# Performance work log

Measured on AMD Instinct MI355X. Metric: run time of the kernel, lower is better.

Reference implementation:

```python
import jax, jax.numpy as jnp
import numpy as np


def _causal_mask(n):
    # pixelSNAIL get_causal_mask: strict lower triangular (pixel i attends to pixels < i)
    return jnp.tril(jnp.ones((n, n), dtype=jnp.float32), k=-1)


def setup_inputs() -> dict:
    key = jax.random.key(0)
    kq, kk, kv = jax.random.split(key, 3)
    B, H, W, C, CM = 32, 32, 32, 128, 256
    return {
        "query": jax.random.normal(kq, (B, H, W, C), dtype=jnp.float32),
        "key": jax.random.normal(kk, (B, H, W, C), dtype=jnp.float32),
        "value": jax.random.normal(kv, (B, H, W, CM), dtype=jnp.float32),
    }


def reference(query, key, value):
    B = query.shape[0]
    C = key.shape[-1]
    CM = value.shape[-1]
    Nk = int(np.prod(key.shape[1:-1]))
    Nq = int(np.prod(query.shape[1:-1]))
    q = query.reshape(B, Nq, C)
    k = key.reshape(B, Nk, C)
    v = value.reshape(B, Nk, CM)
    # raw QK^T (no 1/sqrt(d) scaling in original)
    dot = jnp.einsum('bqc,bkc->bqk', q, k)
    # NON-STANDARD: softmax over full row first, then multiply by strict causal mask
    probs = jax.nn.softmax(dot, axis=-1) * _causal_mask(Nq)[None]
    mixed = jnp.einsum('bqk,bkm->bqm', probs, v)
    return mixed.reshape(query.shape[:-1] + (CM,))
```

## Files before the change

kernel.cpp:

```cpp
#include <hip/hip_runtime.h>


typedef __attribute__((ext_vector_type(8))) short short8;
typedef __attribute__((ext_vector_type(4))) float floatx4;

#define MFMA16(a, b, c) __builtin_amdgcn_mfma_f32_16x16x32_bf16((a), (b), (c), 0, 0, 0)

constexpr int N = 1024, C = 128, CM = 256, BATCH = 32;
constexpr int BM = 64;
constexpr int BN = 32;
constexpr int NT = N / BN;
constexpr int KFRAG = BN * C;
constexpr int VFRAG = BN * CM;

__device__ __forceinline__ unsigned short f2bf(float x) {
    unsigned int u = __float_as_uint(x);
    u += 0x7fffu + ((u >> 16) & 1u);
    return (unsigned short)(u >> 16);
}
__device__ __forceinline__ float bf2f(unsigned short h) {
    return __uint_as_float(((unsigned int)h) << 16);
}
__device__ __forceinline__ uint2 pack4(const unsigned short* s) {
    uint2 u;
    u.x = (unsigned)s[0] | ((unsigned)s[1] << 16);
    u.y = (unsigned)s[2] | ((unsigned)s[3] << 16);
    return u;
}
__device__ __forceinline__ void gl2lds16(const unsigned short* g, unsigned short* l) {
    __builtin_amdgcn_global_load_lds(
        (const __attribute__((address_space(1))) void*)g,
        (__attribute__((address_space(3))) void*)l, 16, 0, 0);
}

__global__ __launch_bounds__(256, 4)
void prep_kernel(const float* __restrict__ kg, const float* __restrict__ vg,
                 unsigned short* __restrict__ khi, unsigned short* __restrict__ klo,
                 unsigned short* __restrict__ vf)
{
    __shared__ __align__(16) unsigned short sKh[KFRAG];
    __shared__ __align__(16) unsigned short sKl[KFRAG];
    __shared__ __align__(16) unsigned short sV[VFRAG];

    const int tid = threadIdx.x;
    const int l = tid & 63, w = tid >> 6;
    const int tile = blockIdx.x, bat = blockIdx.y;
    const int n0 = tile * BN;
    const float* kb = kg + ((size_t)bat * N + n0) * C;
    const float* vb = vg + ((size_t)bat * N + n0) * CM;

#pragma unroll
    for (int it = 0; it < 4; ++it) {
        const int lin = tid + it * 256;
        const float4 x = *(const float4*)(kb + (size_t)lin * 4);
        const int cr = lin >> 1, h = lin & 1;
        const int slot = cr ^ ((cr >> 4) & 7);
        float xs[4] = {x.x, x.y, x.z, x.w};
        unsigned short hi[4], lo[4];
#pragma unroll
        for (int e = 0; e < 4; ++e) {
            unsigned short hb = f2bf(xs[e]);
            hi[e] = hb;
            lo[e] = f2bf(xs[e] - bf2f(hb));
        }
        *(uint2*)(&sKh[slot * 8 + h * 4]) = pack4(hi);
        *(uint2*)(&sKl[slot * 8 + h * 4]) = pack4(lo);
    }

#pragma unroll
    for (int g = 0; g < 2; ++g) {
        const int k0 = g * 16 + w * 4;
        float xa[4][4];
#pragma unroll
        for (int d = 0; d < 4; ++d) {
            const float4 t = *(const float4*)(vb + (size_t)(k0 + d) * CM + l * 4);
            xa[0][d] = t.x; xa[1][d] = t.y; xa[2][d] = t.z; xa[3][d] = t.w;
        }
        const int qq = k0 >> 3, j0 = k0 & 7;
#pragma unroll
        for (int e = 0; e < 4; ++e) {
            const int cm = l * 4 + e;
            const int ct = cm >> 4, rr = cm & 15;
            const int ch = ct * 64 + qq * 16 + rr;
            const int slot = ch ^ ((ch >> 6) & 15);
            unsigned short o[4];
#pragma unroll
            for (int d = 0; d < 4; ++d) o[d] = f2bf(xa[e][d]);
            *(uint2*)(&sV[slot * 8 + j0]) = pack4(o);
        }
    }

    __syncthreads();

    unsigned short* khb = khi + ((size_t)bat * NT + tile) * KFRAG;
    unsigned short* klb = klo + ((size_t)bat * NT + tile) * KFRAG;
    unsigned short* vfb = vf + ((size_t)bat * NT + tile) * VFRAG;

#pragma unroll
    for (int it = 0; it < 2; ++it) {
        const int oc = tid + it * 256;
        const int cr = ((oc & 15) + ((oc >> 8) << 4)) * 16 + ((oc >> 6) & 3) * 4 + ((oc >> 4) & 3);
        const int slot = cr ^ ((cr >> 4) & 7);
        *(uint4*)(khb + (size_t)oc * 8) = *(const uint4*)(&sKh[slot * 8]);
        *(uint4*)(klb + (size_t)oc * 8) = *(const uint4*)(&sKl[slot * 8]);
    }
#pragma unroll
    for (int it = 0; it < 4; ++it) {
        const int oc = tid + it * 256;
        const int slot = oc ^ ((oc >> 6) & 15);
        *(uint4*)(vfb + (size_t)oc * 8) = *(const uint4*)(&sV[slot * 8]);
    }
}

__global__ __launch_bounds__(256, 2)
void attn_kernel(const float* __restrict__ qg, float* __restrict__ og,
                 const unsigned short* __restrict__ khi,
                 const unsigned short* __restrict__ klo,
                 const unsigned short* __restrict__ vf)
{
    __shared__ __align__(16) unsigned short sKhi[2][KFRAG];
    __shared__ __align__(16) unsigned short sKlo[2][KFRAG];
    __shared__ __align__(16) unsigned short sV[2][VFRAG];

    const int tid = threadIdx.x;
    const int w = tid >> 6, ln = tid & 63;
    const int r = ln & 15, qd = ln >> 4;
    const int bat = blockIdx.x;
    const int qt = blockIdx.y;
    const int q0 = qt * BM;

    const float* qb = qg + (size_t)bat * N * C;
    float* ob = og + (size_t)bat * N * CM;
    const unsigned short* khb = khi + (size_t)bat * NT * KFRAG;
    const unsigned short* klb = klo + (size_t)bat * NT * KFRAG;
    const unsigned short* vfb = vf + (size_t)bat * NT * VFRAG;

    short8 qhi[4], qlo[4];
    {
        const float* qr = qb + (size_t)(q0 + w * 16 + r) * C + qd * 8;
#pragma unroll
        for (int ks = 0; ks < 4; ++ks) {
            float4 a = *(const float4*)(qr + ks * 32);
            float4 b = *(const float4*)(qr + ks * 32 + 4);
            float xs[8] = {a.x, a.y, a.z, a.w, b.x, b.y, b.z, b.w};
            short8 h, l;
#pragma unroll
            for (int j = 0; j < 8; ++j) {
                unsigned short hb = f2bf(xs[j]);
                h[j] = (short)hb;
                l[j] = (short)f2bf(xs[j] - bf2f(hb));
            }
            qhi[ks] = h;
            qlo[ks] = l;
        }
    }

    floatx4 oacc[16];
#pragma unroll
    for (int ct = 0; ct < 16; ++ct) oacc[ct] = (floatx4){0.f, 0.f, 0.f, 0.f};
    float lsum = 0.f;
    const int qrow = q0 + w * 16 + r;

    gl2lds16(khb + (size_t)tid * 8,         &sKhi[0][tid * 8]);
    gl2lds16(khb + (size_t)(tid + 256) * 8, &sKhi[0][(tid + 256) * 8]);
    gl2lds16(klb + (size_t)tid * 8,         &sKlo[0][tid * 8]);
    gl2lds16(klb + (size_t)(tid + 256) * 8, &sKlo[0][(tid + 256) * 8]);
#pragma unroll
    for (int i = 0; i < 4; ++i)
        gl2lds16(vfb + (size_t)(tid + i * 256) * 8, &sV[0][(tid + i * 256) * 8]);

    for (int tile = 0; tile < NT; ++tile) {
        const bool pvt = (tile <= 2 * qt + 1);
        const int cb = tile & 1;

        if (tile + 1 < NT) {
            const unsigned short* k1 = khb + (size_t)(tile + 1) * KFRAG;
            const unsigned short* l1 = klb + (size_t)(tile + 1) * KFRAG;
            unsigned short* dh = &sKhi[cb ^ 1][0];
            unsigned short* dl = &sKlo[cb ^ 1][0];
            gl2lds16(k1 + (size_t)tid * 8,         dh + tid * 8);
            gl2lds16(k1 + (size_t)(tid + 256) * 8, dh + (tid + 256) * 8);
            gl2lds16(l1 + (size_t)tid * 8,         dl + tid * 8);
            gl2lds16(l1 + (size_t)(tid + 256) * 8, dl + (tid + 256) * 8);
            if (tile + 1 <= 2 * qt + 1) {
                const unsigned short* vs = vfb + (size_t)(tile + 1) * VFRAG;
                unsigned short* dv = &sV[cb ^ 1][0];
#pragma unroll
                for (int i = 0; i < 4; ++i)
                    gl2lds16(vs + (size_t)(tid + i * 256) * 8, dv + (tid + i * 256) * 8);
                asm volatile("s_waitcnt vmcnt(8)" ::: "memory");
            } else {
                asm volatile("s_waitcnt vmcnt(4)" ::: "memory");
            }
        } else {
            asm volatile("s_waitcnt vmcnt(0)" ::: "memory");
        }
        asm volatile("s_barrier" ::: "memory");

        float pk[8];
#pragma unroll
        for (int t = 0; t < 2; ++t) {
            floatx4 a0 = (floatx4){0.f, 0.f, 0.f, 0.f};
            floatx4 a1 = (floatx4){0.f, 0.f, 0.f, 0.f};
            floatx4 a2 = (floatx4){0.f, 0.f, 0.f, 0.f};
#pragma unroll
            for (int ks = 0; ks < 4; ++ks) {
                short8 bh = *(const short8*)(&sKhi[cb][(((t * 4 + ks) * 64) + ln) * 8]);
                short8 bl = *(const short8*)(&sKlo[cb][(((t * 4 + ks) * 64) + ln) * 8]);
                a0 = MFMA16(bh, qhi[ks], a0);
                a1 = MFMA16(bh, qlo[ks], a1);
                a2 = MFMA16(bl, qhi[ks], a2);
            }
            const int kbase = tile * BN + t * 16 + qd * 4;
#pragma unroll
            for (int rg = 0; rg < 4; ++rg) {
                float s = a0[rg] + a1[rg] + a2[rg];
                float p = __expf(s - 40.0f);
                lsum += p;
                pk[t * 4 + rg] = (kbase + rg < qrow) ? p : 0.0f;
            }
        }

        if (pvt) {
            unsigned int w0, w1, w2, w3;
            asm("v_cvt_pk_bf16_f32 %0, %1, %2" : "=v"(w0) : "v"(pk[0]), "v"(pk[1]));
            asm("v_cvt_pk_bf16_f32 %0, %1, %2" : "=v"(w1) : "v"(pk[2]), "v"(pk[3]));
            asm("v_cvt_pk_bf16_f32 %0, %1, %2" : "=v"(w2) : "v"(pk[4]), "v"(pk[5]));
            asm("v_cvt_pk_bf16_f32 %0, %1, %2" : "=v"(w3) : "v"(pk[6]), "v"(pk[7]));
            asm("v_permlane32_swap_b32 %0, %1" : "+v"(w0), "+v"(w2));
            asm("v_permlane16_swap_b32 %0, %1" : "+v"(w0), "+v"(w2));
            asm("v_permlane32_swap_b32 %0, %1" : "+v"(w1), "+v"(w3));
            asm("v_permlane16_swap_b32 %0, %1" : "+v"(w1), "+v"(w3));
            uint4 apu = make_uint4(w0, w1, w2, w3);
            short8 ap = *(const short8*)&apu;
#pragma unroll
            for (int ct = 0; ct < 16; ++ct) {
                short8 bv = *(const short8*)(&sV[cb][(ct * 64 + ln) * 8]);
                oacc[ct] = MFMA16(ap, bv, oacc[ct]);
            }
        }
        asm volatile("s_barrier" ::: "memory");
    }

    float vtot = lsum;
    vtot += __shfl_xor(vtot, 16);
    vtot += __shfl_xor(vtot, 32);

#pragma unroll
    for (int rg = 0; rg < 4; ++rg) {
        float inv = 1.0f / __shfl(vtot, qd * 4 + rg);
        float* orow = ob + (size_t)(q0 + w * 16 + qd * 4 + rg) * CM;
#pragma unroll
        for (int ct = 0; ct < 16; ++ct)
            orow[ct * 16 + r] = oacc[ct][rg] * inv;
    }
}

extern "C" void kernel_launch(void* const* d_in, const int* in_sizes, int n_in,
                              void* d_out, int out_size, void* d_ws, size_t ws_size,
                              hipStream_t stream) {
    const float* q = (const float*)d_in[0];
    const float* k = (const float*)d_in[1];
    const float* v = (const float*)d_in[2];
    float* o = (float*)d_out;
    (void)n_in; (void)in_sizes; (void)out_size; (void)ws_size;

    unsigned short* khi = (unsigned short*)d_ws;
    unsigned short* klo = khi + (size_t)BATCH * NT * KFRAG;
    unsigned short* vf  = klo + (size_t)BATCH * NT * KFRAG;

    prep_kernel<<<dim3(NT, BATCH), dim3(256), 0, stream>>>(k, v, khi, klo, vf);
    attn_kernel<<<dim3(BATCH, N / BM), dim3(256), 0, stream>>>(q, o, khi, klo, vf);
}
```

Before: 151.6 us.

## Double query rows per wave to reuse K/V LDS fragments across two row groups

Raises the query tile from 64 to 128 rows, giving each wave two 16-row groups. Every K and V fragment read from LDS now feeds two MFMAs, and K/V global traffic per query row is halved because the grid has half as many blocks. The cost is twice the accumulator registers, which forces occupancy down to one block per SIMD group. The grid also drops to 256 blocks, so GPU fill and the tail effects of the causal work imbalance get worse.

New measurement: 164.4 us. +8.4%, slower.

```diff
diff --git a/kernel.cpp b/kernel.cpp
--- a/kernel.cpp
+++ b/kernel.cpp
@@ -7,7 +7,7 @@
 #define MFMA16(a, b, c) __builtin_amdgcn_mfma_f32_16x16x32_bf16((a), (b), (c), 0, 0, 0)
 
 constexpr int N = 1024, C = 128, CM = 256, BATCH = 32;
-constexpr int BM = 64;
+constexpr int BM = 128;
 constexpr int BN = 32;
 constexpr int NT = N / BN;
 constexpr int KFRAG = BN * C;
@@ -112,7 +112,7 @@
     }
 }
 
-__global__ __launch_bounds__(256, 2)
+__global__ __launch_bounds__(256, 1)
 void attn_kernel(const float* __restrict__ qg, float* __restrict__ og,
                  const unsigned short* __restrict__ khi,
                  const unsigned short* __restrict__ klo,
@@ -128,6 +128,7 @@
     const int bat = blockIdx.x;
     const int qt = blockIdx.y;
     const int q0 = qt * BM;
+    const int wrow0 = q0 + w * 32;
 
     const float* qb = qg + (size_t)bat * N * C;
     float* ob = og + (size_t)bat * N * CM;
@@ -135,9 +136,10 @@
     const unsigned short* klb = klo + (size_t)bat * NT * KFRAG;
     const unsigned short* vfb = vf + (size_t)bat * NT * VFRAG;
 
-    short8 qhi[4], qlo[4];
-    {
-        const float* qr = qb + (size_t)(q0 + w * 16 + r) * C + qd * 8;
+    short8 qhi[2][4], qlo[2][4];
+#pragma unroll
+    for (int g = 0; g < 2; ++g) {
+        const float* qr = qb + (size_t)(wrow0 + g * 16 + r) * C + qd * 8;
 #pragma unroll
         for (int ks = 0; ks < 4; ++ks) {
             float4 a = *(const float4*)(qr + ks * 32);
@@ -150,16 +152,19 @@
                 h[j] = (short)hb;
                 l[j] = (short)f2bf(xs[j] - bf2f(hb));
             }
-            qhi[ks] = h;
-            qlo[ks] = l;
-        }
-    }
-
-    floatx4 oacc[16];
-#pragma unroll
-    for (int ct = 0; ct < 16; ++ct) oacc[ct] = (floatx4){0.f, 0.f, 0.f, 0.f};
-    float lsum = 0.f;
-    const int qrow = q0 + w * 16 + r;
+            qhi[g][ks] = h;
+            qlo[g][ks] = l;
+        }
+    }
+
+    floatx4 oacc[2][16];
+#pragma unroll
+    for (int g = 0; g < 2; ++g)
+#pragma unroll
+        for (int ct = 0; ct < 16; ++ct) oacc[g][ct] = (floatx4){0.f, 0.f, 0.f, 0.f};
+    float lsum[2] = {0.f, 0.f};
+    const int qrow0 = wrow0 + r;
+    const int qrow1 = wrow0 + 16 + r;
 
     gl2lds16(khb + (size_t)tid * 8,         &sKhi[0][tid * 8]);
     gl2lds16(khb + (size_t)(tid + 256) * 8, &sKhi[0][(tid + 256) * 8]);
@@ -170,7 +175,7 @@
         gl2lds16(vfb + (size_t)(tid + i * 256) * 8, &sV[0][(tid + i * 256) * 8]);
 
     for (int tile = 0; tile < NT; ++tile) {
-        const bool pvt = (tile <= 2 * qt + 1);
+        const bool pvt = (tile <= 4 * qt + 3);
         const int cb = tile & 1;
 
         if (tile + 1 < NT) {
@@ -182,7 +187,7 @@
             gl2lds16(k1 + (size_t)(tid + 256) * 8, dh + (tid + 256) * 8);
             gl2lds16(l1 + (size_t)tid * 8,         dl + tid * 8);
             gl2lds16(l1 + (size_t)(tid + 256) * 8, dl + (tid + 256) * 8);
-            if (tile + 1 <= 2 * qt + 1) {
+            if (tile + 1 <= 4 * qt + 3) {
                 const unsigned short* vs = vfb + (size_t)(tile + 1) * VFRAG;
                 unsigned short* dv = &sV[cb ^ 1][0];
 #pragma unroll
@@ -197,62 +202,85 @@
         }
         asm volatile("s_barrier" ::: "memory");
 
-        float pk[8];
+        float pk0[8], pk1[8];
 #pragma unroll
         for (int t = 0; t < 2; ++t) {
-            floatx4 a0 = (floatx4){0.f, 0.f, 0.f, 0.f};
-            floatx4 a1 = (floatx4){0.f, 0.f, 0.f, 0.f};
-            floatx4 a2 = (floatx4){0.f, 0.f, 0.f, 0.f};
+            floatx4 a00 = (floatx4){0.f,0.f,0.f,0.f}, a01 = a00, a02 = a00;
+            floatx4 a10 = a00, a11 = a00, a12 = a00;
 #pragma unroll
             for (int ks = 0; ks < 4; ++ks) {
                 short8 bh = *(const short8*)(&sKhi[cb][(((t * 4 + ks) * 64) + ln) * 8]);
                 short8 bl = *(const short8*)(&sKlo[cb][(((t * 4 + ks) * 64) + ln) * 8]);
-                a0 = MFMA16(bh, qhi[ks], a0);
-                a1 = MFMA16(bh, qlo[ks], a1);
-                a2 = MFMA16(bl, qhi[ks], a2);
+                a00 = MFMA16(bh, qhi[0][ks], a00);
+                a10 = MFMA16(bh, qhi[1][ks], a10);
+                a01 = MFMA16(bh, qlo[0][ks], a01);
+                a11 = MFMA16(bh, qlo[1][ks], a11);
+                a02 = MFMA16(bl, qhi[0][ks], a02);
+                a12 = MFMA16(bl, qhi[1][ks], a12);
             }
             const int kbase = tile * BN + t * 16 + qd * 4;
 #pragma unroll
             for (int rg = 0; rg < 4; ++rg) {
-                float s = a0[rg] + a1[rg] + a2[rg];
-                float p = __expf(s - 40.0f);
-                lsum += p;
-                pk[t * 4 + rg] = (kbase + rg < qrow) ? p : 0.0f;
+                float s0 = a00[rg] + a01[rg] + a02[rg];
+                float p0 = __expf(s0 - 40.0f);
+                lsum[0] += p0;
+                pk0[t * 4 + rg] = (kbase + rg < qrow0) ? p0 : 0.0f;
+                float s1 = a10[rg] + a11[rg] + a12[rg];
+                float p1 = __expf(s1 - 40.0f);
+                lsum[1] += p1;
+                pk1[t * 4 + rg] = (kbase + rg < qrow1) ? p1 : 0.0f;
             }
         }
 
         if (pvt) {
-            unsigned int w0, w1, w2, w3;
-            asm("v_cvt_pk_bf16_f32 %0, %1, %2" : "=v"(w0) : "v"(pk[0]), "v"(pk[1]));
-            asm("v_cvt_pk_bf16_f32 %0, %1, %2" : "=v"(w1) : "v"(pk[2]), "v"(pk[3]));
-            asm("v_cvt_pk_bf16_f32 %0, %1, %2" : "=v"(w2) : "v"(pk[4]), "v"(pk[5]));
-            asm("v_cvt_pk_bf16_f32 %0, %1, %2" : "=v"(w3) : "v"(pk[6]), "v"(pk[7]));
-            asm("v_permlane32_swap_b32 %0, %1" : "+v"(w0), "+v"(w2));
-            asm("v_permlane16_swap_b32 %0, %1" : "+v"(w0), "+v"(w2));
-            asm("v_permlane32_swap_b32 %0, %1" : "+v"(w1), "+v"(w3));
-            asm("v_permlane16_swap_b32 %0, %1" : "+v"(w1), "+v"(w3));
-            uint4 apu = make_uint4(w0, w1, w2, w3);
-            short8 ap = *(const short8*)&apu;
+            unsigned int w00, w01, w02, w03, w10, w11, w12, w13;
+            asm("v_cvt_pk_bf16_f32 %0, %1, %2" : "=v"(w00) : "v"(pk0[0]), "v"(pk0[1]));
+            asm("v_cvt_pk_bf16_f32 %0, %1, %2" : "=v"(w01) : "v"(pk0[2]), "v"(pk0[3]));
+            asm("v_cvt_pk_bf16_f32 %0, %1, %2" : "=v"(w02) : "v"(pk0[4]), "v"(pk0[5]));
+            asm("v_cvt_pk_bf16_f32 %0, %1, %2" : "=v"(w03) : "v"(pk0[6]), "v"(pk0[7]));
+            asm("v_permlane32_swap_b32 %0, %1" : "+v"(w00), "+v"(w02));
+            asm("v_permlane16_swap_b32 %0, %1" : "+v"(w00), "+v"(w02));
+            asm("v_permlane32_swap_b32 %0, %1" : "+v"(w01), "+v"(w03));
+            asm("v_permlane16_swap_b32 %0, %1" : "+v"(w01), "+v"(w03));
+            asm("v_cvt_pk_bf16_f32 %0, %1, %2" : "=v"(w10) : "v"(pk1[0]), "v"(pk1[1]));
+            asm("v_cvt_pk_bf16_f32 %0, %1, %2" : "=v"(w11) : "v"(pk1[2]), "v"(pk1[3]));
+            asm("v_cvt_pk_bf16_f32 %0, %1, %2" : "=v"(w12) : "v"(pk1[4]), "v"(pk1[5]));
+            asm("v_cvt_pk_bf16_f32 %0, %1, %2" : "=v"(w13) : "v"(pk1[6]), "v"(pk1[7]));
+            asm("v_permlane32_swap_b32 %0, %1" : "+v"(w10), "+v"(w12));
+            asm("v_permlane16_swap_b32 %0, %1" : "+v"(w10), "+v"(w12));
+            asm("v_permlane32_swap_b32 %0, %1" : "+v"(w11), "+v"(w13));
+            asm("v_permlane16_swap_b32 %0, %1" : "+v"(w11), "+v"(w13));
+            uint4 apu0 = make_uint4(w00, w01, w02, w03);
+            uint4 apu1 = make_uint4(w10, w11, w12, w13);
+            short8 ap0 = *(const short8*)&apu0;
+            short8 ap1 = *(const short8*)&apu1;
 #pragma unroll
             for (int ct = 0; ct < 16; ++ct) {
                 short8 bv = *(const short8*)(&sV[cb][(ct * 64 + ln) * 8]);
-                oacc[ct] = MFMA16(ap, bv, oacc[ct]);
+                oacc[0][ct] = MFMA16(ap0, bv, oacc[0][ct]);
+                oacc[1][ct] = MFMA16(ap1, bv, oacc[1][ct]);
             }
         }
         asm volatile("s_barrier" ::: "memory");
     }
 
-    float vtot = lsum;
-    vtot += __shfl_xor(vtot, 16);
-    vtot += __shfl_xor(vtot, 32);
+    float vt0 = lsum[0], vt1 = lsum[1];
+    vt0 += __shfl_xor(vt0, 16);
+    vt0 += __shfl_xor(vt0, 32);
+    vt1 += __shfl_xor(vt1, 16);
+    vt1 += __shfl_xor(vt1, 32);
 
 #pragma unroll
     for (int rg = 0; rg < 4; ++rg) {
-        float inv = 1.0f / __shfl(vtot, qd * 4 + rg);
-        float* orow = ob + (size_t)(q0 + w * 16 + qd * 4 + rg) * CM;
-#pragma unroll
-        for (int ct = 0; ct < 16; ++ct)
-            orow[ct * 16 + r] = oacc[ct][rg] * inv;
+        float inv0 = 1.0f / __shfl(vt0, qd * 4 + rg);
+        float inv1 = 1.0f / __shfl(vt1, qd * 4 + rg);
+        float* orow0 = ob + (size_t)(wrow0 + qd * 4 + rg) * CM;
+        float* orow1 = ob + (size_t)(wrow0 + 16 + qd * 4 + rg) * CM;
+#pragma unroll
+        for (int ct = 0; ct < 16; ++ct) {
+            orow0[ct * 16 + r] = oacc[0][ct][rg] * inv0;
+            orow1[ct * 16 + r] = oacc[1][ct][rg] * inv1;
+        }
     }
 }
 
```

## Stream K tiles straight into registers and drop the K shared-memory double buffer

Applied to the files above, without the earlier changes.

Each wave now loads its K hi/lo fragments for the next tile directly from global memory into registers, prefetched after the QK MFMAs. This removes the K staging through LDS, halves LDS use and skips the per-tile barrier once the causal PV phase is over. The query-tile mapping is also permuted: blocks 0..7 keep their index and blocks 8..15 are reversed, which changes how heavy and light causal tiles are scheduled. The trade-off is that all four waves fetch the same K data redundantly, and register pressure rises from the 16 prefetched fragments.

Result: slower. 162.9 us (+7.4%).

```diff
diff --git a/kernel.cpp b/kernel.cpp
--- a/kernel.cpp
+++ b/kernel.cpp
@@ -118,15 +118,14 @@
                  const unsigned short* __restrict__ klo,
                  const unsigned short* __restrict__ vf)
 {
-    __shared__ __align__(16) unsigned short sKhi[2][KFRAG];
-    __shared__ __align__(16) unsigned short sKlo[2][KFRAG];
     __shared__ __align__(16) unsigned short sV[2][VFRAG];
 
     const int tid = threadIdx.x;
     const int w = tid >> 6, ln = tid & 63;
     const int r = ln & 15, qd = ln >> 4;
     const int bat = blockIdx.x;
-    const int qt = blockIdx.y;
+    const int by = blockIdx.y;
+    const int qt = (by < 8) ? by : 23 - by;
     const int q0 = qt * BM;
 
     const float* qb = qg + (size_t)bat * N * C;
@@ -161,41 +160,36 @@
     float lsum = 0.f;
     const int qrow = q0 + w * 16 + r;
 
-    gl2lds16(khb + (size_t)tid * 8,         &sKhi[0][tid * 8]);
-    gl2lds16(khb + (size_t)(tid + 256) * 8, &sKhi[0][(tid + 256) * 8]);
-    gl2lds16(klb + (size_t)tid * 8,         &sKlo[0][tid * 8]);
-    gl2lds16(klb + (size_t)(tid + 256) * 8, &sKlo[0][(tid + 256) * 8]);
+    short8 bh[2][4], bl[2][4];
+    const unsigned short* khl = khb + (size_t)ln * 8;
+    const unsigned short* kll = klb + (size_t)ln * 8;
+#pragma unroll
+    for (int t2 = 0; t2 < 2; ++t2)
+#pragma unroll
+        for (int ks = 0; ks < 4; ++ks) {
+            bh[t2][ks] = *(const short8*)(khl + (t2 * 4 + ks) * 512);
+            bl[t2][ks] = *(const short8*)(kll + (t2 * 4 + ks) * 512);
+        }
 #pragma unroll
     for (int i = 0; i < 4; ++i)
         gl2lds16(vfb + (size_t)(tid + i * 256) * 8, &sV[0][(tid + i * 256) * 8]);
-
+    asm volatile("s_waitcnt vmcnt(0)" ::: "memory");
+    asm volatile("s_barrier" ::: "memory");
+
+#pragma unroll 2
     for (int tile = 0; tile < NT; ++tile) {
-        const bool pvt = (tile <= 2 * qt + 1);
         const int cb = tile & 1;
-
-        if (tile + 1 < NT) {
-            const unsigned short* k1 = khb + (size_t)(tile + 1) * KFRAG;
-            const unsigned short* l1 = klb + (size_t)(tile + 1) * KFRAG;
-            unsigned short* dh = &sKhi[cb ^ 1][0];
-            unsigned short* dl = &sKlo[cb ^ 1][0];
-            gl2lds16(k1 + (size_t)tid * 8,         dh + tid * 8);
-            gl2lds16(k1 + (size_t)(tid + 256) * 8, dh + (tid + 256) * 8);
-            gl2lds16(l1 + (size_t)tid * 8,         dl + tid * 8);
-            gl2lds16(l1 + (size_t)(tid + 256) * 8, dl + (tid + 256) * 8);
-            if (tile + 1 <= 2 * qt + 1) {
-                const unsigned short* vs = vfb + (size_t)(tile + 1) * VFRAG;
-                unsigned short* dv = &sV[cb ^ 1][0];
-#pragma unroll
-                for (int i = 0; i < 4; ++i)
-                    gl2lds16(vs + (size_t)(tid + i * 256) * 8, dv + (tid + i * 256) * 8);
-                asm volatile("s_waitcnt vmcnt(8)" ::: "memory");
-            } else {
-                asm volatile("s_waitcnt vmcnt(4)" ::: "memory");
-            }
-        } else {
-            asm volatile("s_waitcnt vmcnt(0)" ::: "memory");
-        }
-        asm volatile("s_barrier" ::: "memory");
+        const bool pvt  = (tile <= 2 * qt + 1);
+        const bool pvtn = (tile + 1 <= 2 * qt + 1);
+
+        if (pvtn) {
+            const unsigned short* vs = vfb + (size_t)(tile + 1) * VFRAG;
+            unsigned short* dv = &sV[cb ^ 1][0];
+#pragma unroll
+            for (int i = 0; i < 4; ++i)
+                gl2lds16(vs + (size_t)(tid + i * 256) * 8, dv + (tid + i * 256) * 8);
+        }
+        asm volatile("" ::: "memory");
 
         float pk[8];
 #pragma unroll
@@ -205,11 +199,9 @@
             floatx4 a2 = (floatx4){0.f, 0.f, 0.f, 0.f};
 #pragma unroll
             for (int ks = 0; ks < 4; ++ks) {
-                short8 bh = *(const short8*)(&sKhi[cb][(((t * 4 + ks) * 64) + ln) * 8]);
-                short8 bl = *(const short8*)(&sKlo[cb][(((t * 4 + ks) * 64) + ln) * 8]);
-                a0 = MFMA16(bh, qhi[ks], a0);
-                a1 = MFMA16(bh, qlo[ks], a1);
-                a2 = MFMA16(bl, qhi[ks], a2);
+                a0 = MFMA16(bh[t][ks], qhi[ks], a0);
+                a1 = MFMA16(bh[t][ks], qlo[ks], a1);
+                a2 = MFMA16(bl[t][ks], qhi[ks], a2);
             }
             const int kbase = tile * BN + t * 16 + qd * 4;
 #pragma unroll
@@ -219,6 +211,18 @@
                 lsum += p;
                 pk[t * 4 + rg] = (kbase + rg < qrow) ? p : 0.0f;
             }
+        }
+
+        if (tile + 1 < NT) {
+            const unsigned short* kh1 = khl + (size_t)(tile + 1) * KFRAG;
+            const unsigned short* kl1 = kll + (size_t)(tile + 1) * KFRAG;
+#pragma unroll
+            for (int t2 = 0; t2 < 2; ++t2)
+#pragma unroll
+                for (int ks = 0; ks < 4; ++ks) {
+                    bh[t2][ks] = *(const short8*)(kh1 + (t2 * 4 + ks) * 512);
+                    bl[t2][ks] = *(const short8*)(kl1 + (t2 * 4 + ks) * 512);
+                }
         }
 
         if (pvt) {
@@ -239,7 +243,11 @@
                 oacc[ct] = MFMA16(ap, bv, oacc[ct]);
             }
         }
-        asm volatile("s_barrier" ::: "memory");
+
+        if (pvtn) {
+            asm volatile("s_waitcnt vmcnt(16)" ::: "memory");
+            asm volatile("s_barrier" ::: "memory");
+        }
     }
 
     float vtot = lsum;
```
